# Optimization experiments

Measured on AMD Instinct MI355X. Metric: run time of the kernel, lower is better.

The kernel has to match this reference:

```python
import jax, jax.numpy as jnp
import numpy as np

D_MODEL = 1024
N_HEADS = 16
D_K = D_MODEL // N_HEADS
SCALE = float(np.sqrt(D_K))


def setup_inputs() -> dict:
    key = jax.random.key(0)
    ks = jax.random.split(key, 11)
    B, L, D = 2, 2048, D_MODEL
    s = 1.0 / np.sqrt(D)
    inp = {
        "q": jax.random.normal(ks[0], (B, L, D), dtype=jnp.float32),
        "k": jax.random.normal(ks[1], (B, L, D), dtype=jnp.float32),
        "v": jax.random.normal(ks[2], (B, L, D), dtype=jnp.float32),
        "Wq": jax.random.normal(ks[3], (D, D), dtype=jnp.float32) * s,
        "bq": jnp.zeros((D,), dtype=jnp.float32),
        "Wk": jax.random.normal(ks[4], (D, D), dtype=jnp.float32) * s,
        "bk": jnp.zeros((D,), dtype=jnp.float32),
        "Wv": jax.random.normal(ks[5], (D, D), dtype=jnp.float32) * s,
        "bv": jnp.zeros((D,), dtype=jnp.float32),
        "Wo": jax.random.normal(ks[6], (D, D), dtype=jnp.float32) * s,
        "bo": jnp.zeros((D,), dtype=jnp.float32),
    }
    return inp


def reference(q, k, v, Wq, bq, Wk, bk, Wv, bv, Wo, bo):
    B, L, D = q.shape
    H, Dk = N_HEADS, D_K
    # projections: [B,L,D] -> [B,H,L,Dk]
    def proj(x, W, b):
        y = x @ W + b
        return y.reshape(B, -1, H, Dk).transpose(0, 2, 1, 3)
    qh = proj(q, Wq, bq)
    kh = proj(k, Wk, bk)
    vh = proj(v, Wv, bv)
    # scores [B,H,Lq,Lk]
    scores = jnp.einsum("bhqd,bhkd->bhqk", qh, kh) / SCALE
    attn = jax.nn.softmax(scores, axis=-1)  # dropout=0.0 -> identity
    out = jnp.einsum("bhqk,bhkd->bhqd", attn, vh)
    out = out.transpose(0, 2, 1, 3).reshape(B, -1, D)
    return out @ Wo + bo
```

## Files before the change

kernel.cpp:

```cpp
#include <hip/hip_runtime.h>
#include <hip/hip_bf16.h>
#include <stdint.h>
#include <stddef.h>

typedef unsigned short ushortT;
typedef __attribute__((ext_vector_type(8))) short bf16x8s;
typedef __attribute__((ext_vector_type(4))) float f32x4;


__device__ __forceinline__ short f2bf(float f) {
  unsigned u = __float_as_uint(f);
  u += 0x7FFFu + ((u >> 16) & 1u);
  return (short)(u >> 16);
}

__device__ __forceinline__ bf16x8s cvt8(const float* src) {
  const float4* p = (const float4*)src;
  float4 a = p[0], b = p[1];
  bf16x8s r;
  r[0] = f2bf(a.x); r[1] = f2bf(a.y); r[2] = f2bf(a.z); r[3] = f2bf(a.w);
  r[4] = f2bf(b.x); r[5] = f2bf(b.y); r[6] = f2bf(b.z); r[7] = f2bf(b.w);
  return r;
}

__device__ __forceinline__ unsigned cvtpk_bf16(float lo, float hi) {
  unsigned r;
  asm("v_cvt_pk_bf16_f32 %0, %1, %2" : "=v"(r) : "v"(lo), "v"(hi));
  return r;
}

__device__ __forceinline__ void load_lds16(const ushortT* g, ushortT* l) {
  __builtin_amdgcn_global_load_lds(
      (const __attribute__((address_space(1))) void*)(g),
      (__attribute__((address_space(3))) void*)(l), 16, 0, 0);
}

__global__ __launch_bounds__(256)
void prep(const float* __restrict__ q, const float* __restrict__ k,
          const float* __restrict__ v,
          const float* __restrict__ Wq, const float* __restrict__ Wk,
          const float* __restrict__ Wv, const float* __restrict__ Wo,
          ushortT* __restrict__ Qc, ushortT* __restrict__ Kc,
          ushortT* __restrict__ Vc, ushortT* __restrict__ Wt)
{
  const int z = blockIdx.z;
  if (z < 4) {
    if (blockIdx.x >= 1024) return;
    __shared__ __align__(16) ushortT t[32][33];
    const float* W = (z == 0) ? Wq : (z == 1) ? Wk : (z == 2) ? Wv : Wo;
    ushortT* dst = Wt + (size_t)z * 1024 * 1024;
    const int x = (blockIdx.x & 31) * 32, y = (blockIdx.x >> 5) * 32;
    const int tx = threadIdx.x & 31, ty = threadIdx.x >> 5;
#pragma unroll
    for (int i = ty; i < 32; i += 8)
      t[i][tx] = (ushortT)f2bf(W[(size_t)(y + i) * 1024 + x + tx]);
    __syncthreads();
#pragma unroll
    for (int i = ty; i < 32; i += 8)
      dst[(size_t)(x + i) * 1024 + y + tx] = t[tx][i];
  } else {
    const float* src = (z == 4) ? q : (z == 5) ? k : v;
    ushortT* dst = (z == 4) ? Qc : (z == 5) ? Kc : Vc;
    const size_t i8 = ((size_t)blockIdx.x * 256 + threadIdx.x) * 8;
    *(bf16x8s*)(dst + i8) = cvt8(src + i8);
  }
}

__device__ __forceinline__ void gemm_core_128(
    const ushortT* __restrict__ A, const ushortT* __restrict__ Bt,
    int K, ushortT* As, ushortT* Bs, f32x4 (&acc)[4][4], int m0, int n0)
{
  const int tid  = threadIdx.x;
  const int wave = tid >> 6, lane = tid & 63;
  const int wm = (wave & 1) << 6;
  const int wn = (wave >> 1) << 6;
  const int lr = lane & 15;
  const int lk = (lane >> 4) << 3;

#pragma unroll
  for (int mi = 0; mi < 4; ++mi)
#pragma unroll
    for (int ni = 0; ni < 4; ++ni)
      acc[mi][ni] = (f32x4){0.f, 0.f, 0.f, 0.f};

  for (int k0 = 0; k0 < K; k0 += 32) {
    __syncthreads();
#pragma unroll
    for (int i = 0; i < 2; ++i) {
      const int cc  = tid + (i << 8);
      const int row = cc >> 2;
      const int ko  = (cc & 3) << 3;
      load_lds16(A  + (size_t)(m0 + row) * K + k0 + ko, As + cc * 8);
      load_lds16(Bt + (size_t)(n0 + row) * K + k0 + ko, Bs + cc * 8);
    }
    __syncthreads();

    bf16x8s af[4], bfr[4];
#pragma unroll
    for (int i = 0; i < 4; ++i)
      af[i] = *(const bf16x8s*)(As + (wm + i * 16 + lr) * 32 + lk);
#pragma unroll
    for (int i = 0; i < 4; ++i)
      bfr[i] = *(const bf16x8s*)(Bs + (wn + i * 16 + lr) * 32 + lk);

#pragma unroll
    for (int mi = 0; mi < 4; ++mi)
#pragma unroll
      for (int ni = 0; ni < 4; ++ni)
        acc[mi][ni] = __builtin_amdgcn_mfma_f32_16x16x32_bf16(
            af[mi], bfr[ni], acc[mi][ni], 0, 0, 0);
  }
}

__global__ __launch_bounds__(256)
void proj_gemm(const ushortT* __restrict__ Qc, const ushortT* __restrict__ Kc,
               const ushortT* __restrict__ Vc, const ushortT* __restrict__ WtAll,
               const float* __restrict__ bq, const float* __restrict__ bk,
               const float* __restrict__ bv,
               ushortT* __restrict__ Qh, ushortT* __restrict__ Kh,
               ushortT* __restrict__ Vt)
{
  __shared__ __align__(16) ushortT As[128 * 32];
  __shared__ __align__(16) ushortT Bs[128 * 32];
  const int which = blockIdx.z;
  const ushortT* A  = (which == 0) ? Qc : (which == 1) ? Kc : Vc;
  const ushortT* Bt = WtAll + (size_t)which * 1024 * 1024;
  const float* bias = (which == 0) ? bq : (which == 1) ? bk : bv;
  const int m0 = blockIdx.x * 128, n0 = blockIdx.y * 128;

  f32x4 acc[4][4];
  gemm_core_128(A, Bt, 1024, As, Bs, acc, m0, n0);

  const int lane = threadIdx.x & 63, wave = threadIdx.x >> 6;
  const int wm = (wave & 1) << 6, wn = (wave >> 1) << 6;
  const int lr = lane & 15, quad = lane >> 4;
  const float QSCALE = 0.18033688011112042f;

#pragma unroll
  for (int ni = 0; ni < 4; ++ni) {
    const int n = n0 + wn + ni * 16 + lr;
    const float bias_v = bias[n];
    const int h = n >> 6, d = n & 63;
#pragma unroll
    for (int mi = 0; mi < 4; ++mi) {
#pragma unroll
      for (int r = 0; r < 4; ++r) {
        const int m = m0 + wm + mi * 16 + quad * 4 + r;
        const int b = m >> 11, l = m & 2047;
        float val = acc[mi][ni][r] + bias_v;
        if (which == 0) val *= QSCALE;
        const ushortT o = (ushortT)f2bf(val);
        const size_t bh = (size_t)(b * 16 + h);
        if (which == 0)      Qh[(bh * 2048 + l) * 64 + d] = o;
        else if (which == 1) Kh[(bh * 2048 + l) * 64 + d] = o;
        else                 Vt[(bh * 64 + d) * 2048 + l] = o;
      }
    }
  }
}

__global__ __launch_bounds__(256)
void attn_kernel(const ushortT* __restrict__ Qh, const ushortT* __restrict__ Kh,
                 const ushortT* __restrict__ Vt, ushortT* __restrict__ Ob)
{
  const int b = blockIdx.z, h = blockIdx.y, qt = blockIdx.x;
  const int bh = b * 16 + h;
  const int wave = threadIdx.x >> 6, lane = threadIdx.x & 63;
  const int lr = lane & 15, quad = lane >> 4, lk = quad * 8;
  const int q0 = qt * 128 + wave * 32;

  const ushortT* Q = Qh + ((size_t)bh * 2048 + q0) * 64;
  const ushortT* K = Kh + (size_t)bh * 2048 * 64;
  const ushortT* V = Vt + (size_t)bh * 64 * 2048;

  __shared__ __align__(16) ushortT Ks[64 * 76];
  __shared__ __align__(16) ushortT Vs[64 * 76];
  __shared__ __align__(16) ushortT P4[4][32 * 84];
  ushortT* Pw = P4[wave];

  bf16x8s qf[2][2];
#pragma unroll
  for (int mt = 0; mt < 2; ++mt) {
    qf[mt][0] = *(const bf16x8s*)(Q + (mt * 16 + lr) * 64 + lk);
    qf[mt][1] = *(const bf16x8s*)(Q + (mt * 16 + lr) * 64 + 32 + lk);
  }

  f32x4 o[2][4];
#pragma unroll
  for (int mt = 0; mt < 2; ++mt)
#pragma unroll
    for (int nt = 0; nt < 4; ++nt) o[mt][nt] = (f32x4){0.f, 0.f, 0.f, 0.f};
  float lsum[2] = {0.f, 0.f};

  const int tid = threadIdx.x;
  const int srow = tid >> 3;
  const int sc8  = (tid & 7) << 3;
  const ushortT* Kg = K + (size_t)srow * 64 + sc8;
  const ushortT* Vg = V + (size_t)srow * 2048 + sc8;

  bf16x8s kch[2], vch[2];
  kch[0] = *(const bf16x8s*)(Kg);
  kch[1] = *(const bf16x8s*)(Kg + 32 * 64);
  vch[0] = *(const bf16x8s*)(Vg);
  vch[1] = *(const bf16x8s*)(Vg + 32 * 2048);

  for (int kt = 0; kt < 2048; kt += 64) {
    __syncthreads();
    *(bf16x8s*)(Ks + srow * 76 + sc8)        = kch[0];
    *(bf16x8s*)(Ks + (srow + 32) * 76 + sc8) = kch[1];
    *(bf16x8s*)(Vs + srow * 76 + sc8)        = vch[0];
    *(bf16x8s*)(Vs + (srow + 32) * 76 + sc8) = vch[1];
    __syncthreads();

    const int ktn = (kt + 64) & 2047;
    kch[0] = *(const bf16x8s*)(Kg + (size_t)ktn * 64);
    kch[1] = *(const bf16x8s*)(Kg + (size_t)(ktn + 32) * 64);
    vch[0] = *(const bf16x8s*)(Vg + ktn);
    vch[1] = *(const bf16x8s*)(Vg + 32 * 2048 + ktn);

    f32x4 s4[2][4];
#pragma unroll
    for (int mt = 0; mt < 2; ++mt)
#pragma unroll
      for (int t = 0; t < 4; ++t) s4[mt][t] = (f32x4){0.f, 0.f, 0.f, 0.f};

    __builtin_amdgcn_s_setprio(1);
#pragma unroll
    for (int t = 0; t < 4; ++t) {
      const bf16x8s kf0 = *(const bf16x8s*)(Ks + (t * 16 + lr) * 76 + lk);
      const bf16x8s kf1 = *(const bf16x8s*)(Ks + (t * 16 + lr) * 76 + 32 + lk);
#pragma unroll
      for (int mt = 0; mt < 2; ++mt) {
        s4[mt][t] = __builtin_amdgcn_mfma_f32_16x16x32_bf16(kf0, qf[mt][0], s4[mt][t], 0, 0, 0);
        s4[mt][t] = __builtin_amdgcn_mfma_f32_16x16x32_bf16(kf1, qf[mt][1], s4[mt][t], 0, 0, 0);
      }
    }
    __builtin_amdgcn_s_setprio(0);

#pragma unroll
    for (int mt = 0; mt < 2; ++mt)
#pragma unroll
      for (int t = 0; t < 4; ++t) {
        const float e0 = __builtin_amdgcn_exp2f(s4[mt][t][0]);
        const float e1 = __builtin_amdgcn_exp2f(s4[mt][t][1]);
        const float e2 = __builtin_amdgcn_exp2f(s4[mt][t][2]);
        const float e3 = __builtin_amdgcn_exp2f(s4[mt][t][3]);
        lsum[mt] += (e0 + e1) + (e2 + e3);
        uint2 d;
        d.x = cvtpk_bf16(e0, e1);
        d.y = cvtpk_bf16(e2, e3);
        *(uint2*)(Pw + (mt * 16 + lr) * 84 + t * 16 + quad * 4) = d;
      }
    asm volatile("s_waitcnt lgkmcnt(0)" ::: "memory");

    bf16x8s pf[2][2];
#pragma unroll
    for (int mt = 0; mt < 2; ++mt) {
      pf[mt][0] = *(const bf16x8s*)(Pw + (mt * 16 + lr) * 84 + lk);
      pf[mt][1] = *(const bf16x8s*)(Pw + (mt * 16 + lr) * 84 + 32 + lk);
    }
    __builtin_amdgcn_s_setprio(1);
#pragma unroll
    for (int nt = 0; nt < 4; ++nt) {
      const bf16x8s vf0 = *(const bf16x8s*)(Vs + (nt * 16 + lr) * 76 + lk);
      const bf16x8s vf1 = *(const bf16x8s*)(Vs + (nt * 16 + lr) * 76 + 32 + lk);
#pragma unroll
      for (int mt = 0; mt < 2; ++mt) {
        o[mt][nt] = __builtin_amdgcn_mfma_f32_16x16x32_bf16(pf[mt][0], vf0, o[mt][nt], 0, 0, 0);
        o[mt][nt] = __builtin_amdgcn_mfma_f32_16x16x32_bf16(pf[mt][1], vf1, o[mt][nt], 0, 0, 0);
      }
    }
    __builtin_amdgcn_s_setprio(0);
  }

  float* fP = (float*)Pw;
#pragma unroll
  for (int mt = 0; mt < 2; ++mt) {
    float s = lsum[mt];
    s += __shfl_xor(s, 16);
    s += __shfl_xor(s, 32);
    fP[mt * 16 + lr] = 1.0f / s;
  }
  asm volatile("s_waitcnt lgkmcnt(0)" ::: "memory");
  float invr[2][4];
#pragma unroll
  for (int mt = 0; mt < 2; ++mt)
#pragma unroll
    for (int r = 0; r < 4; ++r) invr[mt][r] = fP[mt * 16 + quad * 4 + r];

#pragma unroll
  for (int mt = 0; mt < 2; ++mt)
#pragma unroll
    for (int nt = 0; nt < 4; ++nt) {
      const int dcol = h * 64 + nt * 16 + lr;
#pragma unroll
      for (int r = 0; r < 4; ++r) {
        const int l = q0 + mt * 16 + quad * 4 + r;
        Ob[((size_t)b * 2048 + l) * 1024 + dcol] =
            (ushortT)f2bf(o[mt][nt][r] * invr[mt][r]);
      }
    }
}

__global__ __launch_bounds__(256)
void out_gemm(const ushortT* __restrict__ Ob, const ushortT* __restrict__ Wto,
              const float* __restrict__ bo, float* __restrict__ C)
{
  __shared__ __align__(16) ushortT As[128 * 32];
  __shared__ __align__(16) ushortT Bs[64 * 32];
  const int m0 = blockIdx.x * 128, n0 = blockIdx.y * 64;
  const int tid = threadIdx.x;
  const int wave = tid >> 6, lane = tid & 63;
  const int wm = (wave & 1) << 6;
  const int wn = (wave >> 1) << 5;
  const int lr = lane & 15, lk = (lane >> 4) << 3;

  f32x4 acc[4][2];
#pragma unroll
  for (int mi = 0; mi < 4; ++mi)
#pragma unroll
    for (int ni = 0; ni < 2; ++ni) acc[mi][ni] = (f32x4){0.f, 0.f, 0.f, 0.f};

  const int row = tid >> 2;
  const int ko  = (tid & 3) << 3;
  for (int k0 = 0; k0 < 1024; k0 += 32) {
    __syncthreads();
    load_lds16(Ob  + (size_t)(m0 + row) * 1024 + k0 + ko,      As + row * 32 + ko);
    load_lds16(Ob  + (size_t)(m0 + 64 + row) * 1024 + k0 + ko, As + (64 + row) * 32 + ko);
    load_lds16(Wto + (size_t)(n0 + row) * 1024 + k0 + ko,      Bs + row * 32 + ko);
    __syncthreads();

    bf16x8s af[4], bfr[2];
#pragma unroll
    for (int i = 0; i < 4; ++i)
      af[i] = *(const bf16x8s*)(As + (wm + i * 16 + lr) * 32 + lk);
#pragma unroll
    for (int i = 0; i < 2; ++i)
      bfr[i] = *(const bf16x8s*)(Bs + (wn + i * 16 + lr) * 32 + lk);

#pragma unroll
    for (int mi = 0; mi < 4; ++mi)
#pragma unroll
      for (int ni = 0; ni < 2; ++ni)
        acc[mi][ni] = __builtin_amdgcn_mfma_f32_16x16x32_bf16(
            af[mi], bfr[ni], acc[mi][ni], 0, 0, 0);
  }

  const int quad = lane >> 4;
#pragma unroll
  for (int ni = 0; ni < 2; ++ni) {
    const int n = n0 + wn + ni * 16 + lr;
    const float bias_v = bo[n];
#pragma unroll
    for (int mi = 0; mi < 4; ++mi) {
#pragma unroll
      for (int r = 0; r < 4; ++r) {
        const int m = m0 + wm + mi * 16 + quad * 4 + r;
        C[(size_t)m * 1024 + n] = acc[mi][ni][r] + bias_v;
      }
    }
  }
}

extern "C" void kernel_launch(void* const* d_in, const int* in_sizes, int n_in,
                              void* d_out, int out_size, void* d_ws, size_t ws_size,
                              hipStream_t stream) {
  const float* q  = (const float*)d_in[0];
  const float* k  = (const float*)d_in[1];
  const float* v  = (const float*)d_in[2];
  const float* Wq = (const float*)d_in[3];
  const float* bq = (const float*)d_in[4];
  const float* Wk = (const float*)d_in[5];
  const float* bk = (const float*)d_in[6];
  const float* Wv = (const float*)d_in[7];
  const float* bv = (const float*)d_in[8];
  const float* Wo = (const float*)d_in[9];
  const float* bo = (const float*)d_in[10];

  char* ws = (char*)d_ws;
  ushortT* Wt = (ushortT*)(ws);
  ushortT* Qh = (ushortT*)(ws + (size_t)(8  << 20));
  ushortT* Kh = (ushortT*)(ws + (size_t)(16 << 20));
  ushortT* Vt = (ushortT*)(ws + (size_t)(24 << 20));
  ushortT* Qc = (ushortT*)(ws + (size_t)(32 << 20));
  ushortT* Kc = (ushortT*)(ws + (size_t)(40 << 20));
  ushortT* Vc = (ushortT*)(ws + (size_t)(48 << 20));
  ushortT* Ob = Qc;

  prep<<<dim3(2048, 1, 7), 256, 0, stream>>>(q, k, v, Wq, Wk, Wv, Wo,
                                             Qc, Kc, Vc, Wt);
  proj_gemm<<<dim3(32, 8, 3), 256, 0, stream>>>(Qc, Kc, Vc, Wt, bq, bk, bv,
                                                Qh, Kh, Vt);
  attn_kernel<<<dim3(16, 16, 2), 256, 0, stream>>>(Qh, Kh, Vt, Ob);
  out_gemm<<<dim3(32, 16), 256, 0, stream>>>(Ob, Wt + (size_t)3 * 1024 * 1024,
                                             bo, (float*)d_out);
}
```

Baseline: 252.3 us.

## Remap attention block order for XCD locality and drop register prefetch and setprio

```diff
diff --git a/kernel.cpp b/kernel.cpp
--- a/kernel.cpp
+++ b/kernel.cpp
@@ -163,7 +163,9 @@
 void attn_kernel(const ushortT* __restrict__ Qh, const ushortT* __restrict__ Kh,
                  const ushortT* __restrict__ Vt, ushortT* __restrict__ Ob)
 {
-  const int b = blockIdx.z, h = blockIdx.y, qt = blockIdx.x;
+  const int iflat = blockIdx.x + (blockIdx.y << 4) + (blockIdx.z << 8);
+  const int f     = ((iflat & 7) << 6) | (iflat >> 3);
+  const int qt = f & 15, h = (f >> 4) & 15, b = f >> 8;
   const int bh = b * 16 + h;
   const int wave = threadIdx.x >> 6, lane = threadIdx.x & 63;
   const int lr = lane & 15, quad = lane >> 4, lk = quad * 8;
@@ -195,56 +197,48 @@
   const int tid = threadIdx.x;
   const int srow = tid >> 3;
   const int sc8  = (tid & 7) << 3;
-  const ushortT* Kg = K + (size_t)srow * 64 + sc8;
-  const ushortT* Vg = V + (size_t)srow * 2048 + sc8;
-
-  bf16x8s kch[2], vch[2];
-  kch[0] = *(const bf16x8s*)(Kg);
-  kch[1] = *(const bf16x8s*)(Kg + 32 * 64);
-  vch[0] = *(const bf16x8s*)(Vg);
-  vch[1] = *(const bf16x8s*)(Vg + 32 * 2048);
 
   for (int kt = 0; kt < 2048; kt += 64) {
-    __syncthreads();
-    *(bf16x8s*)(Ks + srow * 76 + sc8)        = kch[0];
-    *(bf16x8s*)(Ks + (srow + 32) * 76 + sc8) = kch[1];
-    *(bf16x8s*)(Vs + srow * 76 + sc8)        = vch[0];
-    *(bf16x8s*)(Vs + (srow + 32) * 76 + sc8) = vch[1];
-    __syncthreads();
-
-    const int ktn = (kt + 64) & 2047;
-    kch[0] = *(const bf16x8s*)(Kg + (size_t)ktn * 64);
-    kch[1] = *(const bf16x8s*)(Kg + (size_t)(ktn + 32) * 64);
-    vch[0] = *(const bf16x8s*)(Vg + ktn);
-    vch[1] = *(const bf16x8s*)(Vg + 32 * 2048 + ktn);
-
-    f32x4 s4[2][4];
+    bf16x8s kch[2], vch[2];
+#pragma unroll
+    for (int i = 0; i < 2; ++i) {
+      const int row = srow + i * 32;
+      kch[i] = *(const bf16x8s*)(K + (size_t)(kt + row) * 64 + sc8);
+      vch[i] = *(const bf16x8s*)(V + (size_t)row * 2048 + kt + sc8);
+    }
+    __syncthreads();
+#pragma unroll
+    for (int i = 0; i < 2; ++i) {
+      const int row = srow + i * 32;
+      *(bf16x8s*)(Ks + row * 76 + sc8) = kch[i];
+      *(bf16x8s*)(Vs + row * 76 + sc8) = vch[i];
+    }
+    __syncthreads();
+
+    f32x4 s[2][4];
 #pragma unroll
     for (int mt = 0; mt < 2; ++mt)
 #pragma unroll
-      for (int t = 0; t < 4; ++t) s4[mt][t] = (f32x4){0.f, 0.f, 0.f, 0.f};
-
-    __builtin_amdgcn_s_setprio(1);
+      for (int t = 0; t < 4; ++t) s[mt][t] = (f32x4){0.f, 0.f, 0.f, 0.f};
 #pragma unroll
     for (int t = 0; t < 4; ++t) {
       const bf16x8s kf0 = *(const bf16x8s*)(Ks + (t * 16 + lr) * 76 + lk);
       const bf16x8s kf1 = *(const bf16x8s*)(Ks + (t * 16 + lr) * 76 + 32 + lk);
 #pragma unroll
       for (int mt = 0; mt < 2; ++mt) {
-        s4[mt][t] = __builtin_amdgcn_mfma_f32_16x16x32_bf16(kf0, qf[mt][0], s4[mt][t], 0, 0, 0);
-        s4[mt][t] = __builtin_amdgcn_mfma_f32_16x16x32_bf16(kf1, qf[mt][1], s4[mt][t], 0, 0, 0);
-      }
-    }
-    __builtin_amdgcn_s_setprio(0);
+        s[mt][t] = __builtin_amdgcn_mfma_f32_16x16x32_bf16(kf0, qf[mt][0], s[mt][t], 0, 0, 0);
+        s[mt][t] = __builtin_amdgcn_mfma_f32_16x16x32_bf16(kf1, qf[mt][1], s[mt][t], 0, 0, 0);
+      }
+    }
 
 #pragma unroll
     for (int mt = 0; mt < 2; ++mt)
 #pragma unroll
       for (int t = 0; t < 4; ++t) {
-        const float e0 = __builtin_amdgcn_exp2f(s4[mt][t][0]);
-        const float e1 = __builtin_amdgcn_exp2f(s4[mt][t][1]);
-        const float e2 = __builtin_amdgcn_exp2f(s4[mt][t][2]);
-        const float e3 = __builtin_amdgcn_exp2f(s4[mt][t][3]);
+        const float e0 = __builtin_amdgcn_exp2f(s[mt][t][0]);
+        const float e1 = __builtin_amdgcn_exp2f(s[mt][t][1]);
+        const float e2 = __builtin_amdgcn_exp2f(s[mt][t][2]);
+        const float e3 = __builtin_amdgcn_exp2f(s[mt][t][3]);
         lsum[mt] += (e0 + e1) + (e2 + e3);
         uint2 d;
         d.x = cvtpk_bf16(e0, e1);
@@ -259,7 +253,6 @@
       pf[mt][0] = *(const bf16x8s*)(Pw + (mt * 16 + lr) * 84 + lk);
       pf[mt][1] = *(const bf16x8s*)(Pw + (mt * 16 + lr) * 84 + 32 + lk);
     }
-    __builtin_amdgcn_s_setprio(1);
 #pragma unroll
     for (int nt = 0; nt < 4; ++nt) {
       const bf16x8s vf0 = *(const bf16x8s*)(Vs + (nt * 16 + lr) * 76 + lk);
@@ -270,7 +263,6 @@
         o[mt][nt] = __builtin_amdgcn_mfma_f32_16x16x32_bf16(pf[mt][1], vf1, o[mt][nt], 0, 0, 0);
       }
     }
-    __builtin_amdgcn_s_setprio(0);
   }
 
   float* fP = (float*)Pw;
```

Result: no change. 254.3 us (+0.8%).
